# Optimization experiments

Measured on AMD Instinct MI355X. Metric: run time of the kernel, lower is better.

Reference implementation:

```python
import jax, jax.numpy as jnp
import numpy as np


def setup_inputs() -> dict:
    key = jax.random.key(0)
    k1, k2 = jax.random.split(key)
    inp = jax.random.normal(k1, (4, 2048, 4096), dtype=jnp.float32)
    hra_u = jax.random.normal(k2, (4096, 8), dtype=jnp.float32)
    return {"input": inp, "hra_u": hra_u}


def reference(input, hra_u):
    # HRA forward: out = input @ prod_{i=0..r-1} (I - 2 u_i u_i^T)
    # Applied directly to the input via rank-1 updates (identical math,
    # avoids materializing the d x d delta_weight):
    #   x <- x - 2 (x . u_i) u_i^T, for i = 0..r-1 in order.
    u = hra_u / jnp.linalg.norm(hra_u, axis=0, keepdims=True)  # column-normalize, matches opt_u / opt_u.norm(dim=0)
    x = input
    r = u.shape[1]
    for i in range(r):  # r is small and fixed (8); sequential Householder chain
        ui = u[:, i]                                  # [d]
        proj = jnp.einsum('bsd,d->bs', x, ui)         # [B,S]
        x = x - 2.0 * proj[..., None] * ui            # rank-1 update
    return x
```

## Files before the change

kernel.cpp:

```cpp
#include <hip/hip_runtime.h>

#define D 4096
#define RANK 8
#define BLOCK 1024
#define GRID 256
#define NW (BLOCK / 64)

typedef float f4 __attribute__((ext_vector_type(4)));

__global__ __launch_bounds__(BLOCK, 4) void hra_fused(
    const float* __restrict__ x_in, const float* __restrict__ u_raw,
    float* __restrict__ y, int rows) {
  __shared__ float s_g[NW][36];
  __shared__ float s_G[36];
  __shared__ float s_Gn[64];
  __shared__ float s_T[64];
  __shared__ float s_invn[8];
  __shared__ float s_c[2][2][NW][8];
  __shared__ float s_w[2][2][8];

  const int t = threadIdx.x;
  const int lane = t & 63;
  const int wid = t >> 6;

  float v[4][8];
#pragma unroll
  for (int q = 0; q < 4; ++q) {
    const int d = 4 * t + q;
    const f4* p = (const f4*)(u_raw + (size_t)d * RANK);
    f4 a0 = p[0];
    f4 a1 = p[1];
    v[q][0] = a0.x; v[q][1] = a0.y; v[q][2] = a0.z; v[q][3] = a0.w;
    v[q][4] = a1.x; v[q][5] = a1.y; v[q][6] = a1.z; v[q][7] = a1.w;
  }

  {
    float g[36];
#pragma unroll
    for (int k = 0; k < 36; ++k) g[k] = 0.f;
#pragma unroll
    for (int q = 0; q < 4; ++q) {
      int idx = 0;
#pragma unroll
      for (int i = 0; i < 8; ++i)
#pragma unroll
        for (int j = i; j < 8; ++j)
          g[idx++] += v[q][i] * v[q][j];
    }
#pragma unroll
    for (int off = 32; off >= 1; off >>= 1) {
#pragma unroll
      for (int k = 0; k < 36; ++k)
        g[k] += __shfl_xor(g[k], off, 64);
    }
    if (lane == 0) {
#pragma unroll
      for (int k = 0; k < 36; ++k) s_g[wid][k] = g[k];
    }
  }
  __syncthreads();

  if (t < 36) {
    float s = 0.f;
#pragma unroll
    for (int w2 = 0; w2 < NW; ++w2) s += s_g[w2][t];
    s_G[t] = s;
  }
  __syncthreads();

  if (t < 8) {
    const int dix[8] = {0, 8, 15, 21, 26, 30, 33, 35};
    s_invn[t] = rsqrtf(s_G[dix[t]]);
  }
  __syncthreads();

  if (t < 64) {
    const int i = t >> 3, j = t & 7;
    const int ii = i < j ? i : j;
    const int jj = i < j ? j : i;
    const int idx = ii * 8 - (ii * (ii - 1)) / 2 + (jj - ii);
    s_Gn[t] = s_G[idx] * s_invn[i] * s_invn[j];
  }
  __syncthreads();

  if (t < 8) {
    const int j = t;
    for (int k = 0; k < j; ++k) s_T[k * 8 + j] = 0.f;
    s_T[j * 8 + j] = 2.f;
    for (int k = j + 1; k < 8; ++k) {
      float s = 0.f;
      for (int l = j; l < k; ++l) s += s_Gn[k * 8 + l] * s_T[l * 8 + j];
      s_T[k * 8 + j] = -2.f * s;
    }
  }
  __syncthreads();

  {
    float invn[8];
#pragma unroll
    for (int i = 0; i < 8; ++i) invn[i] = s_invn[i];
#pragma unroll
    for (int q = 0; q < 4; ++q)
#pragma unroll
      for (int i = 0; i < 8; ++i) v[q][i] *= invn[i];
  }
  float Trow[8];
#pragma unroll
  for (int k = 0; k < 8; ++k) Trow[k] = s_T[((t >> 2) & 7) * 8 + k];

  const int rpb = rows / GRID;
  const int npair = rpb / 2;
  const int base = blockIdx.x * rpb;

  f4 nxt0 = *(const f4*)(x_in + (size_t)(base + 0) * D + 4 * t);
  f4 nxt1 = *(const f4*)(x_in + (size_t)(base + 1) * D + 4 * t);
  f4 cur0, cur1, prv0, prv1;

#pragma unroll 2
  for (int p = 0; p < npair; ++p) {
    cur0 = nxt0;
    cur1 = nxt1;
    const float xc0[4] = {cur0.x, cur0.y, cur0.z, cur0.w};
    const float xc1[4] = {cur1.x, cur1.y, cur1.z, cur1.w};

    float acc[2][8];
#pragma unroll
    for (int i = 0; i < 8; ++i) { acc[0][i] = 0.f; acc[1][i] = 0.f; }
#pragma unroll
    for (int q = 0; q < 4; ++q)
#pragma unroll
      for (int i = 0; i < 8; ++i) {
        acc[0][i] += xc0[q] * v[q][i];
        acc[1][i] += xc1[q] * v[q][i];
      }

    const int pn = (p + 1 < npair) ? p + 1 : p;
    nxt0 = *(const f4*)(x_in + (size_t)(base + 2 * pn) * D + 4 * t);
    nxt1 = *(const f4*)(x_in + (size_t)(base + 2 * pn + 1) * D + 4 * t);

#pragma unroll
    for (int off = 32; off >= 1; off >>= 1) {
#pragma unroll
      for (int i = 0; i < 8; ++i) {
        acc[0][i] += __shfl_xor(acc[0][i], off, 64);
        acc[1][i] += __shfl_xor(acc[1][i], off, 64);
      }
    }
    if (lane == 0) {
      f4 a0 = {acc[0][0], acc[0][1], acc[0][2], acc[0][3]};
      f4 a1 = {acc[0][4], acc[0][5], acc[0][6], acc[0][7]};
      f4 b0 = {acc[1][0], acc[1][1], acc[1][2], acc[1][3]};
      f4 b1 = {acc[1][4], acc[1][5], acc[1][6], acc[1][7]};
      *(f4*)&s_c[p & 1][0][wid][0] = a0;
      *(f4*)&s_c[p & 1][0][wid][4] = a1;
      *(f4*)&s_c[p & 1][1][wid][0] = b0;
      *(f4*)&s_c[p & 1][1][wid][4] = b1;
    }

    if (p > 0 && t < 64) {
      const int row = t >> 5;
      const int j = (t >> 2) & 7;
      const int s = t & 3;
      const float* cb = &s_c[(p - 1) & 1][row][0][0];
      f4 cl = *(const f4*)(cb + s * 8) + *(const f4*)(cb + (s + 4) * 8) +
              *(const f4*)(cb + (s + 8) * 8) + *(const f4*)(cb + (s + 12) * 8);
      f4 ch = *(const f4*)(cb + s * 8 + 4) + *(const f4*)(cb + (s + 4) * 8 + 4) +
              *(const f4*)(cb + (s + 8) * 8 + 4) + *(const f4*)(cb + (s + 12) * 8 + 4);
      float wsum = Trow[0] * cl.x + Trow[1] * cl.y + Trow[2] * cl.z +
                   Trow[3] * cl.w + Trow[4] * ch.x + Trow[5] * ch.y +
                   Trow[6] * ch.z + Trow[7] * ch.w;
      wsum += __shfl_xor(wsum, 1, 64);
      wsum += __shfl_xor(wsum, 2, 64);
      if (s == 0) s_w[(p - 1) & 1][row][j] = wsum;
      (void)j;
    }

    __syncthreads();

    if (p > 0) {
      float w0[8], w1[8];
#pragma unroll
      for (int i = 0; i < 8; ++i) {
        w0[i] = s_w[(p - 1) & 1][0][i];
        w1[i] = s_w[(p - 1) & 1][1][i];
      }
      float xp0[4] = {prv0.x, prv0.y, prv0.z, prv0.w};
      float xp1[4] = {prv1.x, prv1.y, prv1.z, prv1.w};
#pragma unroll
      for (int q = 0; q < 4; ++q) {
        float s0 = 0.f, s1 = 0.f;
#pragma unroll
        for (int i = 0; i < 8; ++i) {
          s0 += w0[i] * v[q][i];
          s1 += w1[i] * v[q][i];
        }
        xp0[q] -= s0;
        xp1[q] -= s1;
      }
      f4 o0 = {xp0[0], xp0[1], xp0[2], xp0[3]};
      f4 o1 = {xp1[0], xp1[1], xp1[2], xp1[3]};
      *(f4*)(y + (size_t)(base + 2 * (p - 1)) * D + 4 * t) = o0;
      *(f4*)(y + (size_t)(base + 2 * (p - 1) + 1) * D + 4 * t) = o1;
    }
    prv0 = cur0;
    prv1 = cur1;
  }

  {
    const int pl = npair - 1;
    if (t < 64) {
      const int row = t >> 5;
      const int j = (t >> 2) & 7;
      const int s = t & 3;
      const float* cb = &s_c[pl & 1][row][0][0];
      f4 cl = *(const f4*)(cb + s * 8) + *(const f4*)(cb + (s + 4) * 8) +
              *(const f4*)(cb + (s + 8) * 8) + *(const f4*)(cb + (s + 12) * 8);
      f4 ch = *(const f4*)(cb + s * 8 + 4) + *(const f4*)(cb + (s + 4) * 8 + 4) +
              *(const f4*)(cb + (s + 8) * 8 + 4) + *(const f4*)(cb + (s + 12) * 8 + 4);
      float wsum = Trow[0] * cl.x + Trow[1] * cl.y + Trow[2] * cl.z +
                   Trow[3] * cl.w + Trow[4] * ch.x + Trow[5] * ch.y +
                   Trow[6] * ch.z + Trow[7] * ch.w;
      wsum += __shfl_xor(wsum, 1, 64);
      wsum += __shfl_xor(wsum, 2, 64);
      if (s == 0) s_w[pl & 1][row][j] = wsum;
    }
    __syncthreads();

    float w0[8], w1[8];
#pragma unroll
    for (int i = 0; i < 8; ++i) {
      w0[i] = s_w[pl & 1][0][i];
      w1[i] = s_w[pl & 1][1][i];
    }
    float xp0[4] = {prv0.x, prv0.y, prv0.z, prv0.w};
    float xp1[4] = {prv1.x, prv1.y, prv1.z, prv1.w};
#pragma unroll
    for (int q = 0; q < 4; ++q) {
      float s0 = 0.f, s1 = 0.f;
#pragma unroll
      for (int i = 0; i < 8; ++i) {
        s0 += w0[i] * v[q][i];
        s1 += w1[i] * v[q][i];
      }
      xp0[q] -= s0;
      xp1[q] -= s1;
    }
    f4 o0 = {xp0[0], xp0[1], xp0[2], xp0[3]};
    f4 o1 = {xp1[0], xp1[1], xp1[2], xp1[3]};
    *(f4*)(y + (size_t)(base + 2 * pl) * D + 4 * t) = o0;
    *(f4*)(y + (size_t)(base + 2 * pl + 1) * D + 4 * t) = o1;
  }
}

extern "C" void kernel_launch(void* const* d_in, const int* in_sizes, int n_in,
                              void* d_out, int out_size, void* d_ws, size_t ws_size,
                              hipStream_t stream) {
  const float* x_in = (const float*)d_in[0];
  const float* u = (const float*)d_in[1];
  float* y = (float*)d_out;
  (void)d_ws; (void)ws_size;

  const int rows = in_sizes[0] / D;

  hipLaunchKernelGGL(hra_fused, dim3(GRID), dim3(BLOCK), 0, stream,
                     x_in, u, y, rows);
}
```

Measured before the change: 304.4 us.

## Split fused HRA kernel into setup, dot-product, and apply kernels

Replaces the single persistent fused kernel with three launches. One block precomputes normalized u and the WY-style B = V·T matrix. A highly parallel kernel computes per-row projections C, and a third applies y = x - C·B with nontemporal stores. The aim is to raise memory-level parallelism over the latency-bound 256-block fused loop. The cost is reading the input twice and extra launch and workspace traffic.

```diff
diff --git a/kernel.cpp b/kernel.cpp
--- a/kernel.cpp
+++ b/kernel.cpp
@@ -2,22 +2,18 @@
 
 #define D 4096
 #define RANK 8
-#define BLOCK 1024
-#define GRID 256
-#define NW (BLOCK / 64)
 
 typedef float f4 __attribute__((ext_vector_type(4)));
 
-__global__ __launch_bounds__(BLOCK, 4) void hra_fused(
-    const float* __restrict__ x_in, const float* __restrict__ u_raw,
-    float* __restrict__ y, int rows) {
-  __shared__ float s_g[NW][36];
+
+__global__ __launch_bounds__(1024) void hra_setup(
+    const float* __restrict__ u_raw, float* __restrict__ vn_out,
+    float* __restrict__ B_out) {
+  __shared__ float s_g[16][36];
   __shared__ float s_G[36];
   __shared__ float s_Gn[64];
   __shared__ float s_T[64];
   __shared__ float s_invn[8];
-  __shared__ float s_c[2][2][NW][8];
-  __shared__ float s_w[2][2][8];
 
   const int t = threadIdx.x;
   const int lane = t & 63;
@@ -63,7 +59,7 @@
   if (t < 36) {
     float s = 0.f;
 #pragma unroll
-    for (int w2 = 0; w2 < NW; ++w2) s += s_g[w2][t];
+    for (int w2 = 0; w2 < 16; ++w2) s += s_g[w2][t];
     s_G[t] = s;
   }
   __syncthreads();
@@ -104,151 +100,122 @@
 #pragma unroll
       for (int i = 0; i < 8; ++i) v[q][i] *= invn[i];
   }
-  float Trow[8];
-#pragma unroll
-  for (int k = 0; k < 8; ++k) Trow[k] = s_T[((t >> 2) & 7) * 8 + k];
-
-  const int rpb = rows / GRID;
-  const int npair = rpb / 2;
-  const int base = blockIdx.x * rpb;
-
-  f4 nxt0 = *(const f4*)(x_in + (size_t)(base + 0) * D + 4 * t);
-  f4 nxt1 = *(const f4*)(x_in + (size_t)(base + 1) * D + 4 * t);
-  f4 cur0, cur1, prv0, prv1;
+
+#pragma unroll
+  for (int q = 0; q < 4; ++q) {
+    f4 lo = {v[q][0], v[q][1], v[q][2], v[q][3]};
+    f4 hi = {v[q][4], v[q][5], v[q][6], v[q][7]};
+    f4* p = (f4*)(vn_out + (size_t)(4 * t + q) * RANK);
+    p[0] = lo;
+    p[1] = hi;
+  }
+
+#pragma unroll
+  for (int k = 0; k < 8; ++k) {
+    float Tk[8];
+#pragma unroll
+    for (int j = 0; j < 8; ++j) Tk[j] = s_T[j * 8 + k];
+    f4 b;
+    float bq[4];
+#pragma unroll
+    for (int q = 0; q < 4; ++q) {
+      float s = 0.f;
+#pragma unroll
+      for (int j = 0; j < 8; ++j) s += v[q][j] * Tk[j];
+      bq[q] = s;
+    }
+    b.x = bq[0]; b.y = bq[1]; b.z = bq[2]; b.w = bq[3];
+    *(f4*)(B_out + (size_t)k * D + 4 * t) = b;
+  }
+}
+
+#define K1_BLOCK 256
+__global__ __launch_bounds__(K1_BLOCK) void hra_dots(
+    const float* __restrict__ x_in, const float* __restrict__ vn,
+    float* __restrict__ C, int rows) {
+  const int lane = threadIdx.x & 63;
+  const int wv = blockIdx.x * (K1_BLOCK / 64) + (threadIdx.x >> 6);
+  const int r0 = wv * 2;
+  if (r0 >= rows) return;
+
+  const float* x0 = x_in + (size_t)r0 * D;
+  const float* x1 = x0 + D;
+
+  float acc0[8], acc1[8];
+#pragma unroll
+  for (int i = 0; i < 8; ++i) { acc0[i] = 0.f; acc1[i] = 0.f; }
 
 #pragma unroll 2
-  for (int p = 0; p < npair; ++p) {
-    cur0 = nxt0;
-    cur1 = nxt1;
-    const float xc0[4] = {cur0.x, cur0.y, cur0.z, cur0.w};
-    const float xc1[4] = {cur1.x, cur1.y, cur1.z, cur1.w};
-
-    float acc[2][8];
-#pragma unroll
-    for (int i = 0; i < 8; ++i) { acc[0][i] = 0.f; acc[1][i] = 0.f; }
-#pragma unroll
-    for (int q = 0; q < 4; ++q)
-#pragma unroll
-      for (int i = 0; i < 8; ++i) {
-        acc[0][i] += xc0[q] * v[q][i];
-        acc[1][i] += xc1[q] * v[q][i];
-      }
-
-    const int pn = (p + 1 < npair) ? p + 1 : p;
-    nxt0 = *(const f4*)(x_in + (size_t)(base + 2 * pn) * D + 4 * t);
-    nxt1 = *(const f4*)(x_in + (size_t)(base + 2 * pn + 1) * D + 4 * t);
-
-#pragma unroll
-    for (int off = 32; off >= 1; off >>= 1) {
-#pragma unroll
-      for (int i = 0; i < 8; ++i) {
-        acc[0][i] += __shfl_xor(acc[0][i], off, 64);
-        acc[1][i] += __shfl_xor(acc[1][i], off, 64);
-      }
-    }
-    if (lane == 0) {
-      f4 a0 = {acc[0][0], acc[0][1], acc[0][2], acc[0][3]};
-      f4 a1 = {acc[0][4], acc[0][5], acc[0][6], acc[0][7]};
-      f4 b0 = {acc[1][0], acc[1][1], acc[1][2], acc[1][3]};
-      f4 b1 = {acc[1][4], acc[1][5], acc[1][6], acc[1][7]};
-      *(f4*)&s_c[p & 1][0][wid][0] = a0;
-      *(f4*)&s_c[p & 1][0][wid][4] = a1;
-      *(f4*)&s_c[p & 1][1][wid][0] = b0;
-      *(f4*)&s_c[p & 1][1][wid][4] = b1;
-    }
-
-    if (p > 0 && t < 64) {
-      const int row = t >> 5;
-      const int j = (t >> 2) & 7;
-      const int s = t & 3;
-      const float* cb = &s_c[(p - 1) & 1][row][0][0];
-      f4 cl = *(const f4*)(cb + s * 8) + *(const f4*)(cb + (s + 4) * 8) +
-              *(const f4*)(cb + (s + 8) * 8) + *(const f4*)(cb + (s + 12) * 8);
-      f4 ch = *(const f4*)(cb + s * 8 + 4) + *(const f4*)(cb + (s + 4) * 8 + 4) +
-              *(const f4*)(cb + (s + 8) * 8 + 4) + *(const f4*)(cb + (s + 12) * 8 + 4);
-      float wsum = Trow[0] * cl.x + Trow[1] * cl.y + Trow[2] * cl.z +
-                   Trow[3] * cl.w + Trow[4] * ch.x + Trow[5] * ch.y +
-                   Trow[6] * ch.z + Trow[7] * ch.w;
-      wsum += __shfl_xor(wsum, 1, 64);
-      wsum += __shfl_xor(wsum, 2, 64);
-      if (s == 0) s_w[(p - 1) & 1][row][j] = wsum;
-      (void)j;
-    }
-
-    __syncthreads();
-
-    if (p > 0) {
-      float w0[8], w1[8];
-#pragma unroll
-      for (int i = 0; i < 8; ++i) {
-        w0[i] = s_w[(p - 1) & 1][0][i];
-        w1[i] = s_w[(p - 1) & 1][1][i];
-      }
-      float xp0[4] = {prv0.x, prv0.y, prv0.z, prv0.w};
-      float xp1[4] = {prv1.x, prv1.y, prv1.z, prv1.w};
-#pragma unroll
-      for (int q = 0; q < 4; ++q) {
-        float s0 = 0.f, s1 = 0.f;
-#pragma unroll
-        for (int i = 0; i < 8; ++i) {
-          s0 += w0[i] * v[q][i];
-          s1 += w1[i] * v[q][i];
-        }
-        xp0[q] -= s0;
-        xp1[q] -= s1;
-      }
-      f4 o0 = {xp0[0], xp0[1], xp0[2], xp0[3]};
-      f4 o1 = {xp1[0], xp1[1], xp1[2], xp1[3]};
-      *(f4*)(y + (size_t)(base + 2 * (p - 1)) * D + 4 * t) = o0;
-      *(f4*)(y + (size_t)(base + 2 * (p - 1) + 1) * D + 4 * t) = o1;
-    }
-    prv0 = cur0;
-    prv1 = cur1;
-  }
-
-  {
-    const int pl = npair - 1;
-    if (t < 64) {
-      const int row = t >> 5;
-      const int j = (t >> 2) & 7;
-      const int s = t & 3;
-      const float* cb = &s_c[pl & 1][row][0][0];
-      f4 cl = *(const f4*)(cb + s * 8) + *(const f4*)(cb + (s + 4) * 8) +
-              *(const f4*)(cb + (s + 8) * 8) + *(const f4*)(cb + (s + 12) * 8);
-      f4 ch = *(const f4*)(cb + s * 8 + 4) + *(const f4*)(cb + (s + 4) * 8 + 4) +
-              *(const f4*)(cb + (s + 8) * 8 + 4) + *(const f4*)(cb + (s + 12) * 8 + 4);
-      float wsum = Trow[0] * cl.x + Trow[1] * cl.y + Trow[2] * cl.z +
-                   Trow[3] * cl.w + Trow[4] * ch.x + Trow[5] * ch.y +
-                   Trow[6] * ch.z + Trow[7] * ch.w;
-      wsum += __shfl_xor(wsum, 1, 64);
-      wsum += __shfl_xor(wsum, 2, 64);
-      if (s == 0) s_w[pl & 1][row][j] = wsum;
-    }
-    __syncthreads();
-
-    float w0[8], w1[8];
+  for (int k = 0; k < 16; ++k) {
+    const int d = k * 256 + lane * 4;
+    f4 a = *(const f4*)(x0 + d);
+    f4 b = *(const f4*)(x1 + d);
+    const f4* vp = (const f4*)(vn + (size_t)d * RANK);
+    const float xa[4] = {a.x, a.y, a.z, a.w};
+    const float xb[4] = {b.x, b.y, b.z, b.w};
+#pragma unroll
+    for (int q = 0; q < 4; ++q) {
+      f4 vlo = vp[2 * q];
+      f4 vhi = vp[2 * q + 1];
+      acc0[0] += xa[q] * vlo.x; acc0[1] += xa[q] * vlo.y;
+      acc0[2] += xa[q] * vlo.z; acc0[3] += xa[q] * vlo.w;
+      acc0[4] += xa[q] * vhi.x; acc0[5] += xa[q] * vhi.y;
+      acc0[6] += xa[q] * vhi.z; acc0[7] += xa[q] * vhi.w;
+      acc1[0] += xb[q] * vlo.x; acc1[1] += xb[q] * vlo.y;
+      acc1[2] += xb[q] * vlo.z; acc1[3] += xb[q] * vlo.w;
+      acc1[4] += xb[q] * vhi.x; acc1[5] += xb[q] * vhi.y;
+      acc1[6] += xb[q] * vhi.z; acc1[7] += xb[q] * vhi.w;
+    }
+  }
+
+#pragma unroll
+  for (int off = 32; off >= 1; off >>= 1) {
 #pragma unroll
     for (int i = 0; i < 8; ++i) {
-      w0[i] = s_w[pl & 1][0][i];
-      w1[i] = s_w[pl & 1][1][i];
-    }
-    float xp0[4] = {prv0.x, prv0.y, prv0.z, prv0.w};
-    float xp1[4] = {prv1.x, prv1.y, prv1.z, prv1.w};
-#pragma unroll
-    for (int q = 0; q < 4; ++q) {
-      float s0 = 0.f, s1 = 0.f;
-#pragma unroll
-      for (int i = 0; i < 8; ++i) {
-        s0 += w0[i] * v[q][i];
-        s1 += w1[i] * v[q][i];
-      }
-      xp0[q] -= s0;
-      xp1[q] -= s1;
-    }
-    f4 o0 = {xp0[0], xp0[1], xp0[2], xp0[3]};
-    f4 o1 = {xp1[0], xp1[1], xp1[2], xp1[3]};
-    *(f4*)(y + (size_t)(base + 2 * pl) * D + 4 * t) = o0;
-    *(f4*)(y + (size_t)(base + 2 * pl + 1) * D + 4 * t) = o1;
+      acc0[i] += __shfl_xor(acc0[i], off, 64);
+      acc1[i] += __shfl_xor(acc1[i], off, 64);
+    }
+  }
+
+  if (lane == 0) {
+    f4 c0 = {acc0[0], acc0[1], acc0[2], acc0[3]};
+    f4 c1 = {acc0[4], acc0[5], acc0[6], acc0[7]};
+    f4 c2 = {acc1[0], acc1[1], acc1[2], acc1[3]};
+    f4 c3 = {acc1[4], acc1[5], acc1[6], acc1[7]};
+    f4* cp = (f4*)(C + (size_t)r0 * RANK);
+    cp[0] = c0; cp[1] = c1; cp[2] = c2; cp[3] = c3;
+  }
+}
+
+#define K2_BLOCK 256
+#define K2_ROWS 32
+__global__ __launch_bounds__(K2_BLOCK) void hra_apply(
+    const float* __restrict__ x_in, const float* __restrict__ C,
+    const float* __restrict__ B, float* __restrict__ y, int rows) {
+  const int t = threadIdx.x;
+  const int dq = blockIdx.x & 3;
+  const int rt = blockIdx.x >> 2;
+  const int d = dq * (K2_BLOCK * 4) + 4 * t;
+  const int r0 = rt * K2_ROWS;
+
+  f4 Bk[8];
+#pragma unroll
+  for (int k = 0; k < 8; ++k) Bk[k] = *(const f4*)(B + (size_t)k * D + d);
+
+#pragma unroll 4
+  for (int r = 0; r < K2_ROWS; ++r) {
+    const size_t off = (size_t)(r0 + r) * D + d;
+    f4 x = *(const f4*)(x_in + off);
+    const f4* cp = (const f4*)(C + (size_t)(r0 + r) * RANK);
+    f4 clo = cp[0];
+    f4 chi = cp[1];
+    const float c[8] = {clo.x, clo.y, clo.z, clo.w,
+                        chi.x, chi.y, chi.z, chi.w};
+    f4 s = {0.f, 0.f, 0.f, 0.f};
+#pragma unroll
+    for (int k = 0; k < 8; ++k) s += c[k] * Bk[k];
+    f4 out = x - s;
+    __builtin_nontemporal_store(out, (f4*)(y + off));
   }
 }
 
@@ -258,10 +225,21 @@
   const float* x_in = (const float*)d_in[0];
   const float* u = (const float*)d_in[1];
   float* y = (float*)d_out;
-  (void)d_ws; (void)ws_size;
+  (void)n_in; (void)out_size; (void)ws_size;
 
   const int rows = in_sizes[0] / D;
 
-  hipLaunchKernelGGL(hra_fused, dim3(GRID), dim3(BLOCK), 0, stream,
-                     x_in, u, y, rows);
-}
+  float* vn = (float*)d_ws;
+  float* B = vn + (size_t)D * RANK;
+  float* C = B + (size_t)RANK * D;
+
+  hipLaunchKernelGGL(hra_setup, dim3(1), dim3(1024), 0, stream, u, vn, B);
+
+  const int grid1 = (rows / 2) / (K1_BLOCK / 64);
+  hipLaunchKernelGGL(hra_dots, dim3(grid1), dim3(K1_BLOCK), 0, stream,
+                     x_in, vn, C, rows);
+
+  const int grid2 = (D / (K2_BLOCK * 4)) * (rows / K2_ROWS);
+  hipLaunchKernelGGL(hra_apply, dim3(grid2), dim3(K2_BLOCK), 0, stream,
+                     x_in, C, B, y, rows);
+}
```

New measurement: 340.8 us. 1.12x slower.
